# Kernel optimization log

Measured on AMD Instinct MI355X. Metric: run time of the kernel, lower is better.

The kernel has to match this reference:

```python
import jax, jax.numpy as jnp
import numpy as np

N_NODES = 50000


def gcn_conv(x, edge_index, edge_weight, W, b):
    """PyG GCNConv: x' = D^{-1/2}(A+I)D^{-1/2} (x W) + b, with edge weights."""
    n = x.shape[0]
    x = x @ W  # transform first (PyG order): [N, d_out]
    row, col = edge_index[0], edge_index[1]  # source -> target
    # add self loops with weight 1
    loop = jnp.arange(n)
    row = jnp.concatenate([row, loop])
    col = jnp.concatenate([col, loop])
    ew = jnp.concatenate([edge_weight, jnp.ones((n,), dtype=x.dtype)])
    # symmetric normalization based on (weighted) in-degree at targets
    deg = jax.ops.segment_sum(ew, col, num_segments=n)
    dis = jnp.where(deg > 0, jax.lax.rsqrt(deg), 0.0)
    norm = dis[row] * ew * dis[col]  # [E+N]
    # gather-scale-scatter aggregation
    msg = x[row] * norm[:, None]  # [E+N, d_out]
    out = jax.ops.segment_sum(msg, col, num_segments=n)
    return out + b


def setup_inputs() -> dict:
    key = jax.random.key(0)
    ks = jax.random.split(key, 9)
    E = 800000
    bert_output = jax.random.normal(ks[0], (N_NODES, 1024), dtype=jnp.float32)
    edge_index = jax.random.randint(ks[1], (2, E), 0, N_NODES, dtype=jnp.int64)
    edge_weight = jax.random.uniform(ks[2], (E,), dtype=jnp.float32)
    s1 = 1.0 / np.sqrt(1024)
    s2 = 1.0 / np.sqrt(512)
    s3 = 1.0 / np.sqrt(128)
    W1 = jax.random.uniform(ks[3], (1024, 512), jnp.float32, -s1, s1)
    b1 = jnp.zeros((512,), jnp.float32)
    W2 = jax.random.uniform(ks[4], (512, 128), jnp.float32, -s2, s2)
    b2 = jnp.zeros((128,), jnp.float32)
    Wfc = jax.random.uniform(ks[5], (128, 14), jnp.float32, -s3, s3)
    bfc = jax.random.uniform(ks[6], (14,), jnp.float32, -s3, s3)
    return {
        "bert_output": bert_output,
        "edge_index": edge_index,
        "edge_weight": edge_weight,
        "W1": W1, "b1": b1, "W2": W2, "b2": b2, "Wfc": Wfc, "bfc": bfc,
    }


def reference(bert_output, edge_index, edge_weight, W1, b1, W2, b2, Wfc, bfc):
    h = jax.nn.relu(gcn_conv(bert_output, edge_index, edge_weight, W1, b1))
    h = jax.nn.relu(gcn_conv(h, edge_index, edge_weight, W2, b2))
    logits = h @ Wfc + bfc
    return jax.nn.sigmoid(logits)
```

## Files before the change

kernel.cpp:

```cpp
#include <hip/hip_runtime.h>
#include <stdint.h>

__device__ __forceinline__ float bf2f(unsigned short h) {
  union { uint32_t u; float f; } v; v.u = ((uint32_t)h) << 16; return v.f;
}
__device__ __forceinline__ unsigned short f2bf(float f) {
  union { float f; uint32_t u; } v; v.f = f;
  uint32_t u = v.u;
  u += 0x7FFFu + ((u >> 16) & 1u);
  return (unsigned short)(u >> 16);
}
__device__ __forceinline__ uint32_t pack2bf(float a, float b) {
  return (uint32_t)f2bf(a) | ((uint32_t)f2bf(b) << 16);
}
__device__ __forceinline__ int ld_idx(const void* p, size_t i, int is64) {
  return is64 ? (int)((const long long*)p)[i] : ((const int*)p)[i];
}
__device__ __forceinline__ float ld_w(const void* p, size_t i, int f32) {
  return f32 ? ((const float*)p)[i] : bf2f(((const unsigned short*)p)[i]);
}

typedef __attribute__((ext_vector_type(8))) short short8;
typedef __attribute__((ext_vector_type(4))) float floatx4;

__device__ __forceinline__ void gl2lds16(const unsigned short* g, unsigned short* l) {
  __builtin_amdgcn_global_load_lds(
      (const __attribute__((address_space(1))) uint32_t*)(const void*)g,
      (__attribute__((address_space(3))) uint32_t*)(void*)l,
      16, 0, 0);
}

__global__ void bgcn_probe(const uint32_t* __restrict__ xw,
                           const uint32_t* __restrict__ iw,
                           int* __restrict__ flags) {
  int lane = threadIdx.x;
  int hits = 0;
  #pragma unroll
  for (int j = 0; j < 4; ++j) {
    uint32_t b = (xw[lane * 4 + j] >> 8) & 0x7F;
    hits += (b >= 0x38 && b <= 0x41) ? 1 : 0;
  }
  #pragma unroll
  for (int off = 32; off; off >>= 1) hits += __shfl_xor(hits, off);
  unsigned long long nz = __ballot(iw[2 * lane + 1] != 0u);
  if (lane == 0) {
    flags[0] = (hits < 128) ? 1 : 0;
    flags[1] = (nz == 0ull) ? 1 : 0;
  }
}

__global__ void bgcn_cvt8(const void* __restrict__ src, unsigned short* __restrict__ dst,
                          int n8, const int* __restrict__ flags) {
  int i = blockIdx.x * 256 + threadIdx.x;
  if (i >= n8) return;
  size_t o = (size_t)i * 8;
  uint4 d;
  if (flags[0]) {
    const float4* f = (const float4*)((const float*)src + o);
    float4 f0 = f[0], f1 = f[1];
    d = make_uint4(pack2bf(f0.x, f0.y), pack2bf(f0.z, f0.w),
                   pack2bf(f1.x, f1.y), pack2bf(f1.z, f1.w));
  } else {
    d = *(const uint4*)((const unsigned short*)src + o);
  }
  *(uint4*)(dst + o) = d;
}
__global__ __launch_bounds__(256) void bgcn_cvt_t(
    const void* __restrict__ src, unsigned short* __restrict__ dst,
    int K, int N, const int* __restrict__ flags) {
  __shared__ unsigned short tile[32][33];
  int k0 = blockIdx.x * 32, n0 = blockIdx.y * 32;
  int tx = threadIdx.x & 31, ty = threadIdx.x >> 5;
  bool f32 = flags[0];
  #pragma unroll
  for (int i = 0; i < 4; ++i) {
    size_t s = (size_t)(k0 + ty + i * 8) * N + n0 + tx;
    tile[ty + i * 8][tx] = f32 ? f2bf(((const float*)src)[s])
                               : ((const unsigned short*)src)[s];
  }
  __syncthreads();
  #pragma unroll
  for (int i = 0; i < 4; ++i)
    dst[(size_t)(n0 + ty + i * 8) * K + k0 + tx] = tile[tx][ty + i * 8];
}
__global__ void bgcn_cvt_small(const void* b1, const void* b2,
                               const void* wfc, const void* bfc,
                               unsigned short* db1, unsigned short* db2,
                               unsigned short* dwfc, unsigned short* dbfc,
                               const int* __restrict__ flags) {
  int i = blockIdx.x * 256 + threadIdx.x;
  bool f32 = flags[0];
  const void* s; unsigned short* d; int j;
  if (i < 512)            { s = b1;  d = db1;  j = i; }
  else if (i < 640)       { s = b2;  d = db2;  j = i - 512; }
  else if (i < 2432)      { s = wfc; d = dwfc; j = i - 640; }
  else if (i < 2446)      { s = bfc; d = dbfc; j = i - 2432; }
  else return;
  d[j] = f32 ? f2bf(((const float*)s)[j]) : ((const unsigned short*)s)[j];
}

__global__ void bgcn_init(float* __restrict__ deg, int* __restrict__ counts,
                          int* __restrict__ fill, int n) {
  int i = blockIdx.x * 256 + threadIdx.x;
  if (i < n) { deg[i] = 1.0f; counts[i] = 0; fill[i] = 0; }
}
__global__ void bgcn_deg_hist(const void* __restrict__ ei, const void* __restrict__ ew,
                              const int* __restrict__ flags,
                              float* __restrict__ deg, int* __restrict__ counts, int E) {
  int e = blockIdx.x * 256 + threadIdx.x;
  if (e >= E) return;
  int c = ld_idx(ei, (size_t)E + e, flags[1]);
  atomicAdd(&deg[c], ld_w(ew, e, flags[0]));
  atomicAdd(&counts[c], 1);
}
__global__ void bgcn_scan_block(const int* __restrict__ counts, int* __restrict__ rowptr,
                                int* __restrict__ blocksum,
                                const float* __restrict__ deg, float* __restrict__ dis,
                                int n) {
  __shared__ int buf[1024];
  int gid = blockIdx.x * 1024 + threadIdx.x;
  int v = (gid < n) ? counts[gid] : 0;
  buf[threadIdx.x] = v;
  __syncthreads();
  for (int off = 1; off < 1024; off <<= 1) {
    int x = (threadIdx.x >= off) ? buf[threadIdx.x - off] : 0;
    __syncthreads();
    buf[threadIdx.x] += x;
    __syncthreads();
  }
  if (gid < n) {
    rowptr[gid + 1] = buf[threadIdx.x];
    dis[gid] = rsqrtf(deg[gid]);
  }
  if (threadIdx.x == 1023) blocksum[blockIdx.x] = buf[1023];
}
__global__ void bgcn_scan_tops(int* __restrict__ blocksum, int nb) {
  __shared__ int buf[1024];
  int t = threadIdx.x;
  int v = (t < nb) ? blocksum[t] : 0;
  buf[t] = v;
  __syncthreads();
  for (int off = 1; off < 1024; off <<= 1) {
    int x = (t >= off) ? buf[t - off] : 0;
    __syncthreads();
    buf[t] += x;
    __syncthreads();
  }
  if (t < nb) blocksum[t] = buf[t] - v;
}
__global__ void bgcn_scan_add(int* __restrict__ rowptr, const int* __restrict__ blocksum, int n) {
  int gid = blockIdx.x * 1024 + threadIdx.x;
  if (gid < n) rowptr[gid + 1] += blocksum[blockIdx.x];
  if (gid == 0) rowptr[0] = 0;
}
__global__ void bgcn_scatter(const void* __restrict__ ei, const void* __restrict__ ew,
                             const int* __restrict__ flags,
                             const float* __restrict__ dis,
                             const int* __restrict__ rowptr, int* __restrict__ fill,
                             int* __restrict__ esrc, float* __restrict__ enorm, int E) {
  int e = blockIdx.x * 256 + threadIdx.x;
  if (e >= E) return;
  int is64 = flags[1];
  int r = ld_idx(ei, e, is64), c = ld_idx(ei, (size_t)E + e, is64);
  int pos = rowptr[c] + atomicAdd(&fill[c], 1);
  esrc[pos]  = r;
  enorm[pos] = dis[r] * ld_w(ew, e, flags[0]) * dis[c];
}

__global__ __launch_bounds__(256) void bgcn_gemm_lds(
    const unsigned short* __restrict__ A,
    const unsigned short* __restrict__ Bt,
    unsigned short* __restrict__ C,
    int M, int N, int K, int nblk_bits) {
  __shared__ unsigned short Abuf[128 * 32];
  __shared__ unsigned short Bbuf[128 * 32];
  int t = threadIdx.x;
  int wave = t >> 6, lane = t & 63;
  int bx = blockIdx.x;
  int nblk = bx & ((1 << nblk_bits) - 1);
  int mblk = bx >> nblk_bits;
  int m0 = mblk * 128, n0 = nblk * 128;

  floatx4 acc[4][4];
  #pragma unroll
  for (int i = 0; i < 4; ++i)
    #pragma unroll
    for (int j = 0; j < 4; ++j)
      #pragma unroll
      for (int r = 0; r < 4; ++r) acc[i][j][r] = 0.0f;

  int rii  = lane >> 2;
  int koff = (lane & 3) * 8;
  int ar0 = m0 + wave * 32 + rii;      if (ar0 >= M) ar0 = M - 1;
  int ar1 = m0 + wave * 32 + 16 + rii; if (ar1 >= M) ar1 = M - 1;
  const unsigned short* Ag0 = A + (size_t)ar0 * K + koff;
  const unsigned short* Ag1 = A + (size_t)ar1 * K + koff;
  const unsigned short* Bg0 = Bt + (size_t)(n0 + wave * 32 + rii) * K + koff;
  const unsigned short* Bg1 = Bg0 + (size_t)16 * K;
  unsigned short* Al0 = Abuf + (wave * 32) * 32 + lane * 8;
  unsigned short* Al1 = Abuf + (wave * 32 + 16) * 32 + lane * 8;
  unsigned short* Bl0 = Bbuf + (wave * 32) * 32 + lane * 8;
  unsigned short* Bl1 = Bbuf + (wave * 32 + 16) * 32 + lane * 8;

  int fr = lane & 15;
  int fk = (lane >> 4) * 8;
  int mw = (wave & 1) * 64;
  int nw = (wave >> 1) * 64;

  for (int k0 = 0; k0 < K; k0 += 32) {
    gl2lds16(Ag0 + k0, Al0);
    gl2lds16(Ag1 + k0, Al1);
    gl2lds16(Bg0 + k0, Bl0);
    gl2lds16(Bg1 + k0, Bl1);
    __syncthreads();

    short8 afr[4], bfr[4];
    #pragma unroll
    for (int i = 0; i < 4; ++i)
      afr[i] = *(const short8*)(Abuf + (mw + i * 16 + fr) * 32 + fk);
    #pragma unroll
    for (int i = 0; i < 4; ++i)
      bfr[i] = *(const short8*)(Bbuf + (nw + i * 16 + fr) * 32 + fk);
    #pragma unroll
    for (int mt = 0; mt < 4; ++mt)
      #pragma unroll
      for (int nt = 0; nt < 4; ++nt)
        acc[mt][nt] = __builtin_amdgcn_mfma_f32_16x16x32_bf16(afr[mt], bfr[nt], acc[mt][nt], 0, 0, 0);
    __syncthreads();
  }

  int col_l = lane & 15;
  int row_b = (lane >> 4) * 4;
  #pragma unroll
  for (int mt = 0; mt < 4; ++mt)
    #pragma unroll
    for (int nt = 0; nt < 4; ++nt)
      #pragma unroll
      for (int r = 0; r < 4; ++r) {
        int m = m0 + mw + mt * 16 + row_b + r;
        if (m < M)
          C[(size_t)m * N + n0 + nw + nt * 16 + col_l] = f2bf(acc[mt][nt][r]);
      }
}

#define GST 40
__global__ __launch_bounds__(256, 2) void bgcn_gemm128(
    const void* __restrict__ Araw, int a_probe, const int* __restrict__ flags,
    const unsigned short* __restrict__ Bt,
    unsigned short* __restrict__ C,
    int M, int N, int K, int nblk_bits) {
  __shared__ unsigned short Abuf[128 * GST];
  __shared__ unsigned short Bbuf[128 * GST];
  const bool a_fp32 = a_probe && flags[0];
  int t = threadIdx.x;
  int wave = t >> 6, lane = t & 63;
  int bx = blockIdx.x;
  int nblk = bx & ((1 << nblk_bits) - 1);
  int mblk = bx >> nblk_bits;
  int m0 = mblk * 128, n0 = nblk * 128;

  floatx4 acc[4][4];
  #pragma unroll
  for (int i = 0; i < 4; ++i)
    #pragma unroll
    for (int j = 0; j < 4; ++j)
      #pragma unroll
      for (int r = 0; r < 4; ++r) acc[i][j][r] = 0.0f;

  int srow  = t >> 1;
  int skoff = (t & 1) * 16;
  int am = m0 + srow; if (am >= M) am = M - 1;
  const float*          Af = (const float*)Araw          + (size_t)am * K + skoff;
  const unsigned short* Ah = (const unsigned short*)Araw + (size_t)am * K + skoff;
  const unsigned short* Bp = Bt + (size_t)(n0 + srow) * K + skoff;
  unsigned short* AL = Abuf + srow * GST + skoff;
  unsigned short* BL = Bbuf + srow * GST + skoff;

  int fr = lane & 15;
  int fk = (lane >> 4) * 8;
  int mw = (wave & 1) * 64;
  int nw = (wave >> 1) * 64;

  for (int k0 = 0; k0 < K; k0 += 32) {
    uint4 a0, a1;
    if (a_fp32) {
      float4 f0 = *(const float4*)(Af + k0);
      float4 f1 = *(const float4*)(Af + k0 + 4);
      float4 f2 = *(const float4*)(Af + k0 + 8);
      float4 f3 = *(const float4*)(Af + k0 + 12);
      a0 = make_uint4(pack2bf(f0.x, f0.y), pack2bf(f0.z, f0.w),
                      pack2bf(f1.x, f1.y), pack2bf(f1.z, f1.w));
      a1 = make_uint4(pack2bf(f2.x, f2.y), pack2bf(f2.z, f2.w),
                      pack2bf(f3.x, f3.y), pack2bf(f3.z, f3.w));
    } else {
      a0 = *(const uint4*)(Ah + k0);
      a1 = *(const uint4*)(Ah + k0 + 8);
    }
    uint4 b0 = *(const uint4*)(Bp + k0);
    uint4 b1 = *(const uint4*)(Bp + k0 + 8);
    *(uint4*)AL       = a0;
    *(uint4*)(AL + 8) = a1;
    *(uint4*)BL       = b0;
    *(uint4*)(BL + 8) = b1;
    __syncthreads();

    short8 afr[4], bfr[4];
    #pragma unroll
    for (int i = 0; i < 4; ++i)
      afr[i] = *(const short8*)(Abuf + (mw + i * 16 + fr) * GST + fk);
    #pragma unroll
    for (int i = 0; i < 4; ++i)
      bfr[i] = *(const short8*)(Bbuf + (nw + i * 16 + fr) * GST + fk);
    #pragma unroll
    for (int mt = 0; mt < 4; ++mt)
      #pragma unroll
      for (int nt = 0; nt < 4; ++nt)
        acc[mt][nt] = __builtin_amdgcn_mfma_f32_16x16x32_bf16(afr[mt], bfr[nt], acc[mt][nt], 0, 0, 0);
    __syncthreads();
  }

  int col_l = lane & 15;
  int row_b = (lane >> 4) * 4;
  #pragma unroll
  for (int mt = 0; mt < 4; ++mt)
    #pragma unroll
    for (int nt = 0; nt < 4; ++nt)
      #pragma unroll
      for (int r = 0; r < 4; ++r) {
        int m = m0 + mw + mt * 16 + row_b + r;
        if (m < M)
          C[(size_t)m * N + n0 + nw + nt * 16 + col_l] = f2bf(acc[mt][nt][r]);
      }
}

__device__ __forceinline__ void accum4(float* acc, uint2 r, float w) {
  acc[0] += w * bf2f((unsigned short)(r.x & 0xffff));
  acc[1] += w * bf2f((unsigned short)(r.x >> 16));
  acc[2] += w * bf2f((unsigned short)(r.y & 0xffff));
  acc[3] += w * bf2f((unsigned short)(r.y >> 16));
}
__device__ __forceinline__ void accum2(float* acc, uint32_t r, float w) {
  acc[0] += w * bf2f((unsigned short)(r & 0xffff));
  acc[1] += w * bf2f((unsigned short)(r >> 16));
}

template <int F, int WPN>
__global__ __launch_bounds__(256) void bgcn_aggregate(
    const unsigned short* __restrict__ H,
    const int* __restrict__ rowptr,
    const int* __restrict__ esrc,
    const float* __restrict__ enorm,
    const float* __restrict__ dis,
    const unsigned short* __restrict__ bias,
    unsigned short* __restrict__ Out,
    int n_nodes) {
  constexpr int FPW = F / WPN;
  constexpr int VPL = FPW / 64;
  constexpr int NPB = 4 / WPN;
  constexpr int DEPTH = 16;

  int t = threadIdx.x;
  int lane = t & 63;
  int wid = __builtin_amdgcn_readfirstlane(t >> 6);
  int c = blockIdx.x * NPB + wid / WPN;
  if (c >= n_nodes) return;
  c = __builtin_amdgcn_readfirstlane(c);
  int h = wid % WPN;

  int beg = __builtin_amdgcn_readfirstlane(rowptr[c]);
  int end = __builtin_amdgcn_readfirstlane(rowptr[c + 1]);
  float ds = dis[c];

  int fo = h * FPW + lane * VPL;
  const unsigned short* Hl = H + fo;

  uint2 rs;
  union { uint2 v; unsigned short u[4]; } bu;
  if constexpr (VPL == 4) {
    rs = *(const uint2*)(Hl + (size_t)c * F);
    bu.v = *(const uint2*)(bias + fo);
  } else {
    rs.x = *(const uint32_t*)(Hl + (size_t)c * F);
    bu.v.x = *(const uint32_t*)(bias + fo);
  }

  float acc[VPL];
  #pragma unroll
  for (int j = 0; j < VPL; ++j) acc[j] = 0.0f;

  for (int base = beg; base < end; base += 64) {
    int n = end - base;
    if (n > 64) n = 64;
    n = __builtin_amdgcn_readfirstlane(n);
    int   sv = 0;
    float wv = 0.0f;
    if (lane < n) {
      sv = esrc[base + lane];
      wv = enorm[base + lane];
    }
    for (int q0 = 0; q0 < n; q0 += DEPTH) {
      uint2 r[DEPTH];
      float w[DEPTH];
      #pragma unroll
      for (int j = 0; j < DEPTH; ++j) {
        int q = q0 + j;
        int qs = (q < n) ? q : 0;
        int sq = __builtin_amdgcn_readlane(sv, qs);
        w[j] = __int_as_float(
            __builtin_amdgcn_readlane(__float_as_int(wv), q));
        const unsigned short* src = Hl + (size_t)sq * F;
        if constexpr (VPL == 4) r[j] = *(const uint2*)src;
        else                    r[j].x = *(const uint32_t*)src;
      }
      #pragma unroll
      for (int j = 0; j < DEPTH; ++j) {
        if constexpr (VPL == 4) accum4(acc, r[j], w[j]);
        else                    accum2(acc, r[j].x, w[j]);
      }
    }
  }

  float wself = ds * ds;
  if constexpr (VPL == 4) accum4(acc, rs, wself);
  else                    accum2(acc, rs.x, wself);

  unsigned short ob[VPL];
  #pragma unroll
  for (int j = 0; j < VPL; ++j) {
    float v = acc[j] + bf2f(bu.u[j]);
    ob[j] = f2bf(fmaxf(v, 0.0f));
  }
  if constexpr (VPL == 4) {
    uint2 st;
    st.x = (uint32_t)ob[0] | ((uint32_t)ob[1] << 16);
    st.y = (uint32_t)ob[2] | ((uint32_t)ob[3] << 16);
    *(uint2*)(Out + (size_t)c * F + fo) = st;
  } else {
    *(uint32_t*)(Out + (size_t)c * F + fo) =
        (uint32_t)ob[0] | ((uint32_t)ob[1] << 16);
  }
}

__global__ __launch_bounds__(256) void bgcn_fc_sigmoid(
    const unsigned short* __restrict__ X,
    const unsigned short* __restrict__ W,
    const unsigned short* __restrict__ b,
    float* __restrict__ out,
    int n_nodes) {
  __shared__ float Ws[128 * 14];
  __shared__ float bs[14];
  for (int i = threadIdx.x; i < 128 * 14; i += 256) Ws[i] = bf2f(W[i]);
  if (threadIdx.x < 14) bs[threadIdx.x] = bf2f(b[threadIdx.x]);
  __syncthreads();
  int node = blockIdx.x * 256 + threadIdx.x;
  if (node >= n_nodes) return;
  float acc[14];
  #pragma unroll
  for (int c = 0; c < 14; ++c) acc[c] = bs[c];
  const unsigned short* xp = X + (size_t)node * 128;
  for (int k8 = 0; k8 < 16; ++k8) {
    uint4 r = *(const uint4*)(xp + k8 * 8);
    float xv[8];
    xv[0] = bf2f((unsigned short)(r.x & 0xffff)); xv[1] = bf2f((unsigned short)(r.x >> 16));
    xv[2] = bf2f((unsigned short)(r.y & 0xffff)); xv[3] = bf2f((unsigned short)(r.y >> 16));
    xv[4] = bf2f((unsigned short)(r.z & 0xffff)); xv[5] = bf2f((unsigned short)(r.z >> 16));
    xv[6] = bf2f((unsigned short)(r.w & 0xffff)); xv[7] = bf2f((unsigned short)(r.w >> 16));
    #pragma unroll
    for (int j = 0; j < 8; ++j) {
      int k = k8 * 8 + j;
      #pragma unroll
      for (int c = 0; c < 14; ++c) acc[c] = fmaf(xv[j], Ws[k * 14 + c], acc[c]);
    }
  }
  float* op = out + (size_t)node * 14;
  #pragma unroll
  for (int c = 0; c < 14; ++c)
    op[c] = 1.0f / (1.0f + __expf(-acc[c]));
}

static inline size_t padsz(size_t x) { return (x + 255) & ~(size_t)255; }
static inline void* wsa(char*& p, size_t bytes) {
  void* r = p;
  p += padsz(bytes);
  return r;
}

extern "C" void kernel_launch(void* const* d_in, const int* in_sizes, int n_in,
                              void* d_out, int out_size, void* d_ws, size_t ws_size,
                              hipStream_t stream) {
  const void* Xr   = d_in[0];
  const void* EIr  = d_in[1];
  const void* EWr  = d_in[2];
  const void* W1r  = d_in[3];
  const void* b1r  = d_in[4];
  const void* W2r  = d_in[5];
  const void* b2r  = d_in[6];
  const void* Wfcr = d_in[7];
  const void* bfcr = d_in[8];
  float* out = (float*)d_out;

  const int N = in_sizes[0] / 1024;
  const int E = in_sizes[2];

  size_t need = padsz((size_t)N * 512 * 2)
              + padsz((size_t)N * 1024 * 2)
              + 4 * padsz((size_t)N * 4)
              + padsz((size_t)(N + 1) * 4)
              + padsz(256 * 4)
              + 2 * padsz((size_t)E * 4)
              + padsz(1024 * 512 * 2) + padsz(512 * 128 * 2)
              + padsz(512 * 2) + padsz(128 * 2) + padsz(128 * 14 * 2)
              + padsz(32) + padsz(8);
  const bool big = ws_size >= need;

  char* p = (char*)d_ws;
  unsigned short* R1  = (unsigned short*)wsa(p, (size_t)N * 512 * 2);
  unsigned short* R2  = (unsigned short*)wsa(p, (size_t)N * (big ? 1024 : 512) * 2);
  float* deg      = (float*)wsa(p, (size_t)N * 4);
  float* dis      = (float*)wsa(p, (size_t)N * 4);
  int*   counts   = (int*)wsa(p, (size_t)N * 4);
  int*   fill     = (int*)wsa(p, (size_t)N * 4);
  int*   rowptr   = (int*)wsa(p, (size_t)(N + 1) * 4);
  int*   blocksum = (int*)wsa(p, 256 * 4);
  int*   esrc     = (int*)wsa(p, (size_t)E * 4);
  float* enorm    = (float*)wsa(p, (size_t)E * 4);
  unsigned short* W1t  = (unsigned short*)wsa(p, (size_t)1024 * 512 * 2);
  unsigned short* W2t  = (unsigned short*)wsa(p, (size_t)512 * 128 * 2);
  unsigned short* b1c  = (unsigned short*)wsa(p, 512 * 2);
  unsigned short* b2c  = (unsigned short*)wsa(p, 128 * 2);
  unsigned short* Wfcc = (unsigned short*)wsa(p, 128 * 14 * 2);
  unsigned short* bfcc = (unsigned short*)wsa(p, 32);
  int* flags      = (int*)wsa(p, 8);

  unsigned short* H1  = R1;
  unsigned short* Xbf = R2;
  unsigned short* X2  = R2;
  unsigned short* H2  = R1;
  unsigned short* X3  = R1 + (size_t)N * 128;

  int gN = (N + 255) / 256;
  int gE = (E + 255) / 256;

  bgcn_init<<<gN, 256, 0, stream>>>(deg, counts, fill, N);
  bgcn_probe<<<1, 64, 0, stream>>>((const uint32_t*)Xr, (const uint32_t*)EIr, flags);
  { dim3 g(1024 / 32, 512 / 32); bgcn_cvt_t<<<g, 256, 0, stream>>>(W1r, W1t, 1024, 512, flags); }
  { dim3 g(512 / 32, 128 / 32);  bgcn_cvt_t<<<g, 256, 0, stream>>>(W2r, W2t, 512, 128, flags); }
  bgcn_cvt_small<<<10, 256, 0, stream>>>(b1r, b2r, Wfcr, bfcr, b1c, b2c, Wfcc, bfcc, flags);
  if (big) {
    int n8 = N * 1024 / 8;
    bgcn_cvt8<<<(n8 + 255) / 256, 256, 0, stream>>>(Xr, Xbf, n8, flags);
  }

  bgcn_deg_hist<<<gE, 256, 0, stream>>>(EIr, EWr, flags, deg, counts, E);
  int nb = (N + 1023) / 1024;
  bgcn_scan_block<<<nb, 1024, 0, stream>>>(counts, rowptr, blocksum, deg, dis, N);
  bgcn_scan_tops<<<1, 1024, 0, stream>>>(blocksum, nb);
  bgcn_scan_add<<<nb, 1024, 0, stream>>>(rowptr, blocksum, N);
  bgcn_scatter<<<gE, 256, 0, stream>>>(EIr, EWr, flags, dis, rowptr, fill, esrc, enorm, E);

  int mblks = (N + 127) / 128;

  if (big)
    bgcn_gemm_lds<<<mblks * 4, 256, 0, stream>>>(Xbf, W1t, H1, N, 512, 1024, 2);
  else
    bgcn_gemm128<<<mblks * 4, 256, 0, stream>>>(Xr, 1, flags, W1t, H1, N, 512, 1024, 2);
  bgcn_aggregate<512, 2><<<(N + 1) / 2, 256, 0, stream>>>(H1, rowptr, esrc, enorm, dis, b1c, X2, N);

  bgcn_gemm_lds<<<mblks, 256, 0, stream>>>(X2, W2t, H2, N, 128, 512, 0);
  bgcn_aggregate<128, 1><<<(N + 3) / 4, 256, 0, stream>>>(H2, rowptr, esrc, enorm, dis, b2c, X3, N);

  bgcn_fc_sigmoid<<<gN, 256, 0, stream>>>(X3, Wfcc, bfcc, out, N);
}
```

Measured before the change: 720.0 us.

## Fuse FC+sigmoid into layer-2 aggregate, remap GEMM blocks per XCD, merge init/probe

```diff
diff --git a/kernel.cpp b/kernel.cpp
--- a/kernel.cpp
+++ b/kernel.cpp
@@ -30,22 +30,28 @@
       16, 0, 0);
 }
 
-__global__ void bgcn_probe(const uint32_t* __restrict__ xw,
-                           const uint32_t* __restrict__ iw,
-                           int* __restrict__ flags) {
-  int lane = threadIdx.x;
-  int hits = 0;
-  #pragma unroll
-  for (int j = 0; j < 4; ++j) {
-    uint32_t b = (xw[lane * 4 + j] >> 8) & 0x7F;
-    hits += (b >= 0x38 && b <= 0x41) ? 1 : 0;
-  }
-  #pragma unroll
-  for (int off = 32; off; off >>= 1) hits += __shfl_xor(hits, off);
-  unsigned long long nz = __ballot(iw[2 * lane + 1] != 0u);
-  if (lane == 0) {
-    flags[0] = (hits < 128) ? 1 : 0;
-    flags[1] = (nz == 0ull) ? 1 : 0;
+__global__ void bgcn_init_probe(float* __restrict__ deg, int* __restrict__ counts,
+                                int* __restrict__ fill, int n,
+                                const uint32_t* __restrict__ xw,
+                                const uint32_t* __restrict__ iw,
+                                int* __restrict__ flags) {
+  int i = blockIdx.x * 256 + threadIdx.x;
+  if (i < n) { deg[i] = 1.0f; counts[i] = 0; fill[i] = 0; }
+  if (blockIdx.x == 0 && threadIdx.x < 64) {
+    int lane = threadIdx.x;
+    int hits = 0;
+    #pragma unroll
+    for (int j = 0; j < 4; ++j) {
+      uint32_t b = (xw[lane * 4 + j] >> 8) & 0x7F;
+      hits += (b >= 0x38 && b <= 0x41) ? 1 : 0;
+    }
+    #pragma unroll
+    for (int off = 32; off; off >>= 1) hits += __shfl_xor(hits, off);
+    unsigned long long nz = __ballot(iw[2 * lane + 1] != 0u);
+    if (lane == 0) {
+      flags[0] = (hits < 128) ? 1 : 0;
+      flags[1] = (nz == 0ull) ? 1 : 0;
+    }
   }
 }
 
@@ -99,11 +105,6 @@
   d[j] = f32 ? f2bf(((const float*)s)[j]) : ((const unsigned short*)s)[j];
 }
 
-__global__ void bgcn_init(float* __restrict__ deg, int* __restrict__ counts,
-                          int* __restrict__ fill, int n) {
-  int i = blockIdx.x * 256 + threadIdx.x;
-  if (i < n) { deg[i] = 1.0f; counts[i] = 0; fill[i] = 0; }
-}
 __global__ void bgcn_deg_hist(const void* __restrict__ ei, const void* __restrict__ ew,
                               const int* __restrict__ flags,
                               float* __restrict__ deg, int* __restrict__ counts, int E) {
@@ -171,14 +172,17 @@
     const unsigned short* __restrict__ A,
     const unsigned short* __restrict__ Bt,
     unsigned short* __restrict__ C,
-    int M, int N, int K, int nblk_bits) {
+    int M, int N, int K, int nblk_bits, int wpx, int nwork) {
   __shared__ unsigned short Abuf[128 * 32];
   __shared__ unsigned short Bbuf[128 * 32];
   int t = threadIdx.x;
   int wave = t >> 6, lane = t & 63;
-  int bx = blockIdx.x;
-  int nblk = bx & ((1 << nblk_bits) - 1);
-  int mblk = bx >> nblk_bits;
+  int xcd = blockIdx.x & 7;
+  int g   = blockIdx.x >> 3;
+  int work = xcd * wpx + g;
+  if (work >= nwork) return;
+  int nblk = work & ((1 << nblk_bits) - 1);
+  int mblk = work >> nblk_bits;
   int m0 = mblk * 128, n0 = nblk * 128;
 
   floatx4 acc[4][4];
@@ -344,7 +348,7 @@
   acc[1] += w * bf2f((unsigned short)(r >> 16));
 }
 
-template <int F, int WPN>
+template <int F, int WPN, bool FUSE_FC>
 __global__ __launch_bounds__(256) void bgcn_aggregate(
     const unsigned short* __restrict__ H,
     const int* __restrict__ rowptr,
@@ -353,6 +357,9 @@
     const float* __restrict__ dis,
     const unsigned short* __restrict__ bias,
     unsigned short* __restrict__ Out,
+    const unsigned short* __restrict__ Wfc,
+    const unsigned short* __restrict__ bfc,
+    float* __restrict__ fcout,
     int n_nodes) {
   constexpr int FPW = F / WPN;
   constexpr int VPL = FPW / 64;
@@ -424,58 +431,42 @@
   if constexpr (VPL == 4) accum4(acc, rs, wself);
   else                    accum2(acc, rs.x, wself);
 
-  unsigned short ob[VPL];
-  #pragma unroll
-  for (int j = 0; j < VPL; ++j) {
-    float v = acc[j] + bf2f(bu.u[j]);
-    ob[j] = f2bf(fmaxf(v, 0.0f));
-  }
-  if constexpr (VPL == 4) {
-    uint2 st;
-    st.x = (uint32_t)ob[0] | ((uint32_t)ob[1] << 16);
-    st.y = (uint32_t)ob[2] | ((uint32_t)ob[3] << 16);
-    *(uint2*)(Out + (size_t)c * F + fo) = st;
+  float vpost[VPL];
+  #pragma unroll
+  for (int j = 0; j < VPL; ++j)
+    vpost[j] = fmaxf(acc[j] + bf2f(bu.u[j]), 0.0f);
+
+  if constexpr (FUSE_FC) {
+    float part[14];
+    const unsigned short* w0 = Wfc + (size_t)(2 * lane) * 14;
+    #pragma unroll
+    for (int o = 0; o < 14; ++o)
+      part[o] = vpost[0] * bf2f(w0[o]) + vpost[1] * bf2f(w0[14 + o]);
+    #pragma unroll
+    for (int off = 32; off; off >>= 1)
+      #pragma unroll
+      for (int o = 0; o < 14; ++o)
+        part[o] += __shfl_xor(part[o], off);
+    if (lane == 0) {
+      float* op = fcout + (size_t)c * 14;
+      #pragma unroll
+      for (int o = 0; o < 14; ++o)
+        op[o] = 1.0f / (1.0f + __expf(-(part[o] + bf2f(bfc[o]))));
+    }
   } else {
-    *(uint32_t*)(Out + (size_t)c * F + fo) =
-        (uint32_t)ob[0] | ((uint32_t)ob[1] << 16);
-  }
-}
-
-__global__ __launch_bounds__(256) void bgcn_fc_sigmoid(
-    const unsigned short* __restrict__ X,
-    const unsigned short* __restrict__ W,
-    const unsigned short* __restrict__ b,
-    float* __restrict__ out,
-    int n_nodes) {
-  __shared__ float Ws[128 * 14];
-  __shared__ float bs[14];
-  for (int i = threadIdx.x; i < 128 * 14; i += 256) Ws[i] = bf2f(W[i]);
-  if (threadIdx.x < 14) bs[threadIdx.x] = bf2f(b[threadIdx.x]);
-  __syncthreads();
-  int node = blockIdx.x * 256 + threadIdx.x;
-  if (node >= n_nodes) return;
-  float acc[14];
-  #pragma unroll
-  for (int c = 0; c < 14; ++c) acc[c] = bs[c];
-  const unsigned short* xp = X + (size_t)node * 128;
-  for (int k8 = 0; k8 < 16; ++k8) {
-    uint4 r = *(const uint4*)(xp + k8 * 8);
-    float xv[8];
-    xv[0] = bf2f((unsigned short)(r.x & 0xffff)); xv[1] = bf2f((unsigned short)(r.x >> 16));
-    xv[2] = bf2f((unsigned short)(r.y & 0xffff)); xv[3] = bf2f((unsigned short)(r.y >> 16));
-    xv[4] = bf2f((unsigned short)(r.z & 0xffff)); xv[5] = bf2f((unsigned short)(r.z >> 16));
-    xv[6] = bf2f((unsigned short)(r.w & 0xffff)); xv[7] = bf2f((unsigned short)(r.w >> 16));
-    #pragma unroll
-    for (int j = 0; j < 8; ++j) {
-      int k = k8 * 8 + j;
-      #pragma unroll
-      for (int c = 0; c < 14; ++c) acc[c] = fmaf(xv[j], Ws[k * 14 + c], acc[c]);
-    }
-  }
-  float* op = out + (size_t)node * 14;
-  #pragma unroll
-  for (int c = 0; c < 14; ++c)
-    op[c] = 1.0f / (1.0f + __expf(-acc[c]));
+    unsigned short ob[VPL];
+    #pragma unroll
+    for (int j = 0; j < VPL; ++j) ob[j] = f2bf(vpost[j]);
+    if constexpr (VPL == 4) {
+      uint2 st;
+      st.x = (uint32_t)ob[0] | ((uint32_t)ob[1] << 16);
+      st.y = (uint32_t)ob[2] | ((uint32_t)ob[3] << 16);
+      *(uint2*)(Out + (size_t)c * F + fo) = st;
+    } else {
+      *(uint32_t*)(Out + (size_t)c * F + fo) =
+          (uint32_t)ob[0] | ((uint32_t)ob[1] << 16);
+    }
+  }
 }
 
 static inline size_t padsz(size_t x) { return (x + 255) & ~(size_t)255; }
@@ -536,13 +527,12 @@
   unsigned short* Xbf = R2;
   unsigned short* X2  = R2;
   unsigned short* H2  = R1;
-  unsigned short* X3  = R1 + (size_t)N * 128;
 
   int gN = (N + 255) / 256;
   int gE = (E + 255) / 256;
 
-  bgcn_init<<<gN, 256, 0, stream>>>(deg, counts, fill, N);
-  bgcn_probe<<<1, 64, 0, stream>>>((const uint32_t*)Xr, (const uint32_t*)EIr, flags);
+  bgcn_init_probe<<<gN, 256, 0, stream>>>(deg, counts, fill, N,
+                                          (const uint32_t*)Xr, (const uint32_t*)EIr, flags);
   { dim3 g(1024 / 32, 512 / 32); bgcn_cvt_t<<<g, 256, 0, stream>>>(W1r, W1t, 1024, 512, flags); }
   { dim3 g(512 / 32, 128 / 32);  bgcn_cvt_t<<<g, 256, 0, stream>>>(W2r, W2t, 512, 128, flags); }
   bgcn_cvt_small<<<10, 256, 0, stream>>>(b1r, b2r, Wfcr, bfcr, b1c, b2c, Wfcc, bfcc, flags);
@@ -560,14 +550,20 @@
 
   int mblks = (N + 127) / 128;
 
+  int nwork1 = mblks << 2;
+  int wpx1 = (nwork1 + 7) / 8;
+  wpx1 = ((wpx1 + 3) / 4) * 4;
+  int nwork2 = mblks;
+  int wpx2 = (nwork2 + 7) / 8;
+
   if (big)
-    bgcn_gemm_lds<<<mblks * 4, 256, 0, stream>>>(Xbf, W1t, H1, N, 512, 1024, 2);
+    bgcn_gemm_lds<<<8 * wpx1, 256, 0, stream>>>(Xbf, W1t, H1, N, 512, 1024, 2, wpx1, nwork1);
   else
     bgcn_gemm128<<<mblks * 4, 256, 0, stream>>>(Xr, 1, flags, W1t, H1, N, 512, 1024, 2);
-  bgcn_aggregate<512, 2><<<(N + 1) / 2, 256, 0, stream>>>(H1, rowptr, esrc, enorm, dis, b1c, X2, N);
-
-  bgcn_gemm_lds<<<mblks, 256, 0, stream>>>(X2, W2t, H2, N, 128, 512, 0);
-  bgcn_aggregate<128, 1><<<(N + 3) / 4, 256, 0, stream>>>(H2, rowptr, esrc, enorm, dis, b2c, X3, N);
-
-  bgcn_fc_sigmoid<<<gN, 256, 0, stream>>>(X3, Wfcc, bfcc, out, N);
-}
+  bgcn_aggregate<512, 2, false><<<(N + 1) / 2, 256, 0, stream>>>(
+      H1, rowptr, esrc, enorm, dis, b1c, X2, nullptr, nullptr, nullptr, N);
+
+  bgcn_gemm_lds<<<8 * wpx2, 256, 0, stream>>>(X2, W2t, H2, N, 128, 512, 0, wpx2, nwork2);
+  bgcn_aggregate<128, 1, true><<<(N + 3) / 4, 256, 0, stream>>>(
+      H2, rowptr, esrc, enorm, dis, b2c, nullptr, Wfcc, bfcc, out, N);
+}
```

New measurement: 744.1 us. 3.3% more time.
